# Kernel optimization log

Measured on AMD Instinct MI355X. Metric: run time of the kernel, lower is better.

The kernel has to match this reference:

```python
import jax, jax.numpy as jnp
import numpy as np

N_NODES = 100000
EMB_DIM = 128
HIDDEN = 128
N_EDGES = 1600000
N_LABEL = 200000


def _xavier(key, shape):
    fan_in, fan_out = shape[1], shape[0]
    lim = float(np.sqrt(6.0 / (fan_in + fan_out)))
    return jax.random.uniform(key, shape, jnp.float32, -lim, lim)


def setup_inputs() -> dict:
    key = jax.random.key(0)
    ks = jax.random.split(key, 8)
    n_id = jnp.arange(N_NODES, dtype=jnp.int64) if jax.config.jax_enable_x64 else jnp.arange(N_NODES, dtype=jnp.int32)
    edge_index = jax.random.randint(ks[0], (2, N_EDGES), 0, N_NODES)
    edge_label_index = jax.random.randint(ks[1], (2, N_LABEL), 0, N_NODES)
    emb_weight = _xavier(ks[2], (N_NODES, EMB_DIM))
    # layer 0: in=EMB_DIM -> HIDDEN ; layer 1: HIDDEN -> HIDDEN
    Wl0 = _xavier(ks[3], (HIDDEN, EMB_DIM))
    bl0 = jnp.zeros((HIDDEN,), jnp.float32)
    Wr0 = _xavier(ks[4], (HIDDEN, EMB_DIM))
    Wl1 = _xavier(ks[5], (HIDDEN, HIDDEN))
    bl1 = jnp.zeros((HIDDEN,), jnp.float32)
    Wr1 = _xavier(ks[6], (HIDDEN, HIDDEN))
    return {
        "n_id": n_id,
        "edge_index": edge_index,
        "edge_label_index": edge_label_index,
        "emb_weight": emb_weight,
        "Wl0": Wl0, "bl0": bl0, "Wr0": Wr0,
        "Wl1": Wl1, "bl1": bl1, "Wr1": Wr1,
    }


def _sage_conv(x, src, dst, Wl, bl, Wr, num_nodes):
    # PyG SAGEConv (aggr='mean'): out = lin_l(mean_{j in N(i)} x_j) + lin_r(x_i)
    agg = jax.ops.segment_sum(x[src], dst, num_segments=num_nodes)  # [N, D]
    deg = jax.ops.segment_sum(jnp.ones((src.shape[0],), x.dtype), dst, num_segments=num_nodes)
    mean = agg / jnp.maximum(deg, 1.0)[:, None]
    return mean @ Wl.T + bl + x @ Wr.T


def reference(n_id, edge_index, edge_label_index, emb_weight, Wl0, bl0, Wr0, Wl1, bl1, Wr1):
    src, dst = edge_index[0], edge_index[1]
    num_nodes = n_id.shape[0]
    x = emb_weight[n_id]                                  # [N, EMB_DIM]
    x = _sage_conv(x, src, dst, Wl0, bl0, Wr0, num_nodes)  # layer 0
    x = jax.nn.relu(x)                                     # relu between layers (dropout p=0, eval)
    z = _sage_conv(x, src, dst, Wl1, bl1, Wr1, num_nodes)  # layer 1 (no relu after last)
    s, d = edge_label_index[0], edge_label_index[1]
    return jnp.sum(z[s] * z[d], axis=-1)                   # [N_LABEL]
```

## Files before the change

### kernel.cpp

```cpp
#include <hip/hip_runtime.h>
#include <hip/hip_bf16.h>

typedef short bf16x8 __attribute__((ext_vector_type(8)));
typedef float f32x4 __attribute__((ext_vector_type(4)));
typedef float f32x2 __attribute__((ext_vector_type(2)));

#define BKT_SHIFT 9
#define BKT_RANGE 512
#define MAXBKT 256

__device__ __forceinline__ float bf2f(unsigned short u){
  union { unsigned int i; float f; } v; v.i = ((unsigned int)u)<<16; return v.f;
}
__device__ __forceinline__ unsigned short f2bf(float f){
  union { float f; unsigned int i; } v; v.f = f;
  unsigned int i = v.i;
  return (unsigned short)((i + 0x7fffu + ((i>>16)&1u)) >> 16);
}
__device__ __forceinline__ f32x2 up2(unsigned int v){
  union { unsigned int i; float f; } lo, hi;
  lo.i = v << 16; hi.i = v & 0xffff0000u;
  return (f32x2){lo.f, hi.f};
}

__global__ void k_zero(int* p, int n){
  int i = blockIdx.x*256 + threadIdx.x;
  if(i<n) p[i] = 0;
}

__global__ void k_bcount(const int* dst, int* gcount, int ne, int nbk){
  __shared__ int cnt[MAXBKT];
  int tid = threadIdx.x;
  if(tid < nbk) cnt[tid] = 0;
  __syncthreads();
  int base = blockIdx.x * 4096;
#pragma unroll
  for(int i=0;i<16;++i){
    int e = base + i*256 + tid;
    if(e < ne) atomicAdd(&cnt[dst[e] >> BKT_SHIFT], 1);
  }
  __syncthreads();
  if(tid < nbk && cnt[tid] > 0) atomicAdd(&gcount[tid], cnt[tid]);
}

__global__ void k_bscan(const int* gcount, int* gbase, int* gcursor, int nbk){
  __shared__ int sm[256];
  int t = threadIdx.x;
  int v = (t<nbk) ? gcount[t] : 0;
  sm[t] = v;
  __syncthreads();
  for(int off=1; off<256; off<<=1){
    int a = (t>=off) ? sm[t-off] : 0;
    __syncthreads();
    sm[t] += a;
    __syncthreads();
  }
  if(t<nbk){
    int excl = sm[t] - v;
    gbase[t] = excl;
    gcursor[t] = excl;
  }
}

__global__ void k_bscatter(const int* src, const int* dst, int* gcursor,
                           int2* ebuf, int ne, int nbk){
  __shared__ int cnt[MAXBKT];
  __shared__ int runbase[MAXBKT];
  int tid = threadIdx.x;
  if(tid < nbk) cnt[tid] = 0;
  __syncthreads();
  int base = blockIdx.x * 4096;
  int se[16], de[16], re[16];
#pragma unroll
  for(int i=0;i<16;++i){
    int e = base + i*256 + tid;
    if(e < ne){
      de[i] = dst[e];
      se[i] = src[e];
      re[i] = atomicAdd(&cnt[de[i] >> BKT_SHIFT], 1);
    } else de[i] = -1;
  }
  __syncthreads();
  if(tid < nbk) runbase[tid] = cnt[tid] ? atomicAdd(&gcursor[tid], cnt[tid]) : 0;
  __syncthreads();
#pragma unroll
  for(int i=0;i<16;++i){
    if(de[i] >= 0){
      int pos = runbase[de[i] >> BKT_SHIFT] + re[i];
      ebuf[pos] = make_int2(se[i], de[i]);
    }
  }
}

__global__ void k_bsort(const int2* ebuf, const int* gbase, const int* gcursor,
                        int* csr, int* row_off, int n, int ne, int nbk){
  __shared__ int h[BKT_RANGE];
  __shared__ int cur[BKT_RANGE];
  int t = threadIdx.x;
  int k = blockIdx.x;
  int lo = k << BKT_SHIFT;
  int beg = gbase[k], end = gcursor[k];
  h[t] = 0;
  __syncthreads();
  for(int e = beg + t; e < end; e += 512)
    atomicAdd(&h[ebuf[e].y - lo], 1);
  __syncthreads();
  int v = h[t];
  __shared__ int sm[512];
  sm[t] = v;
  __syncthreads();
  for(int off=1; off<512; off<<=1){
    int a = (t>=off) ? sm[t-off] : 0;
    __syncthreads();
    sm[t] += a;
    __syncthreads();
  }
  int excl = beg + sm[t] - v;
  cur[t] = excl;
  if(lo + t < n) row_off[lo + t] = excl;
  if(k == nbk-1 && t == 0) row_off[n] = ne;
  __syncthreads();
  for(int e = beg + t; e < end; e += 512){
    int2 sd = ebuf[e];
    int pos = atomicAdd(&cur[sd.y - lo], 1);
    csr[pos] = sd.x;
  }
}

__global__ void k_prep(const float* emb, const int* n_id, unsigned short* A0,
                       const float* Wl0, const float* Wr0, unsigned short* wc0,
                       const float* Wl1, const float* Wr1, unsigned short* wc1,
                       int n){
  int b = blockIdx.x;
  if(b < 256){
    const float* Wl = (b < 128) ? Wl0 : Wl1;
    const float* Wr = (b < 128) ? Wr0 : Wr1;
    unsigned short* wc = (b < 128) ? wc0 : wc1;
    int i = (b & 127)*256 + threadIdx.x;
    int nn = i >> 8, k = i & 255;
    float v = (k<128) ? Wl[nn*128 + k] : Wr[nn*128 + k - 128];
    wc[i] = f2bf(v);
  } else {
    int gid = (b-256)*256 + threadIdx.x;
    int row = gid >> 5, c4 = (gid & 31) * 4;
    if(row >= n) return;
    float4 v = *(const float4*)&emb[(long)n_id[row]*128 + c4];
    ushort4 o;
    o.x = f2bf(v.x); o.y = f2bf(v.y); o.z = f2bf(v.z); o.w = f2bf(v.w);
    *(ushort4*)&A0[(long)row*256 + 128 + c4] = o;
  }
}

__global__ void k_agg(const unsigned short* X, unsigned short* Mout,
                      const int* row_off, const int* csr, int n){
  int w = __builtin_amdgcn_readfirstlane((int)((blockIdx.x*blockDim.x + threadIdx.x) >> 6));
  int lane = threadIdx.x & 63;
  if(w >= n) return;
  int beg = row_off[w], end = row_off[w+1];
  int deg = end - beg;
  f32x2 acc = {0.f, 0.f};
  const char* Xb = (const char*)X + 256;
  int e = beg;
  for(; e + 8 <= end; e += 8){
    unsigned int v0 = ((const unsigned int*)(Xb + (long)csr[e  ]*512))[lane];
    unsigned int v1 = ((const unsigned int*)(Xb + (long)csr[e+1]*512))[lane];
    unsigned int v2 = ((const unsigned int*)(Xb + (long)csr[e+2]*512))[lane];
    unsigned int v3 = ((const unsigned int*)(Xb + (long)csr[e+3]*512))[lane];
    unsigned int v4 = ((const unsigned int*)(Xb + (long)csr[e+4]*512))[lane];
    unsigned int v5 = ((const unsigned int*)(Xb + (long)csr[e+5]*512))[lane];
    unsigned int v6 = ((const unsigned int*)(Xb + (long)csr[e+6]*512))[lane];
    unsigned int v7 = ((const unsigned int*)(Xb + (long)csr[e+7]*512))[lane];
    acc += up2(v0); acc += up2(v1); acc += up2(v2); acc += up2(v3);
    acc += up2(v4); acc += up2(v5); acc += up2(v6); acc += up2(v7);
  }
  for(; e + 4 <= end; e += 4){
    unsigned int v0 = ((const unsigned int*)(Xb + (long)csr[e  ]*512))[lane];
    unsigned int v1 = ((const unsigned int*)(Xb + (long)csr[e+1]*512))[lane];
    unsigned int v2 = ((const unsigned int*)(Xb + (long)csr[e+2]*512))[lane];
    unsigned int v3 = ((const unsigned int*)(Xb + (long)csr[e+3]*512))[lane];
    acc += up2(v0); acc += up2(v1); acc += up2(v2); acc += up2(v3);
  }
  for(; e < end; ++e){
    unsigned int v = ((const unsigned int*)(Xb + (long)csr[e]*512))[lane];
    acc += up2(v);
  }
  float inv = (deg>0) ? 1.0f/(float)deg : 0.f;
  float a0 = acc[0]*inv, a1 = acc[1]*inv;
  unsigned int o = ((unsigned int)f2bf(a1) << 16) | (unsigned int)f2bf(a0);
  *(unsigned int*)((char*)Mout + (long)w*512 + lane*4) = o;
}

template<int RELU, int OUTSTRIDE, int OUTOFF>
__global__ __launch_bounds__(256,2) void k_gemm(const unsigned short* A,
                                                const unsigned short* wc,
                                                const float* bias,
                                                unsigned short* out, int nrows){
  __shared__ unsigned short Wl[32768];
  int tid = threadIdx.x;
  for(int it=0; it<16; ++it){
    int idx  = it*256 + tid;
    int byte = idx*16;
    int row  = byte >> 9;
    int swz  = byte ^ ((row & 7) << 4);
    *(uint4*)((char*)Wl + swz) = *(const uint4*)((const char*)wc + byte);
  }
  __syncthreads();

  int lane = tid & 63, wv = tid >> 6;
  float bs[8];
#pragma unroll
  for(int nf=0; nf<8; ++nf) bs[nf] = bias[nf*16 + (lane & 15)];

  for(int t=0; t<4; ++t){
    int rowA = blockIdx.x*256 + t*64 + wv*16 + (lane & 15);
    int rcl  = rowA < nrows ? rowA : nrows-1;
    const char* Ab = (const char*)(A + (long)rcl*256) + ((lane>>4)*16);
    bf16x8 a[8];
#pragma unroll
    for(int k=0;k<8;++k) a[k] = *(const bf16x8*)(Ab + k*64);

    f32x4 acc[8];
#pragma unroll
    for(int i=0;i<8;++i) acc[i] = (f32x4){0.f,0.f,0.f,0.f};

#pragma unroll
    for(int nf=0; nf<8; ++nf){
      int rw = nf*16 + (lane & 15);
#pragma unroll
      for(int k=0;k<8;++k){
        int byte = (rw*512 + k*64 + (lane>>4)*16) ^ ((rw & 7) << 4);
        bf16x8 b = *(const bf16x8*)((const char*)Wl + byte);
        acc[nf] = __builtin_amdgcn_mfma_f32_16x16x32_bf16(a[k], b, acc[nf], 0, 0, 0);
      }
    }

    int rbase = blockIdx.x*256 + t*64 + wv*16 + (lane>>4)*4;
#pragma unroll
    for(int nf=0; nf<8; ++nf){
      int col = nf*16 + (lane & 15);
#pragma unroll
      for(int r=0;r<4;++r){
        int row = rbase + r;
        if(row < nrows){
          float v = acc[nf][r] + bs[nf];
          if(RELU) v = v > 0.f ? v : 0.f;
          out[(long)row*OUTSTRIDE + OUTOFF + col] = f2bf(v);
        }
      }
    }
  }
}

__global__ void k_dot(const unsigned short* z, const int* s, const int* d,
                      float* out, int nl){
  int wv = (blockIdx.x*256 + threadIdx.x) >> 6;
  int lane = threadIdx.x & 63;
  int g = lane >> 4;
  int gl = lane & 15;
  int pi = wv*4 + g;
  float acc = 0.f;
  if(pi < nl){
    int si = s[pi], di = d[pi];
    bf16x8 va = *(const bf16x8*)&z[(long)si*128 + gl*8];
    bf16x8 vb = *(const bf16x8*)&z[(long)di*128 + gl*8];
#pragma unroll
    for(int i=0;i<8;++i)
      acc += bf2f((unsigned short)va[i]) * bf2f((unsigned short)vb[i]);
#pragma unroll
    for(int off=1; off<16; off<<=1)
      acc += __shfl_xor(acc, off, 16);
    if(gl==0) out[pi] = acc;
  }
}

extern "C" void kernel_launch(void* const* d_in, const int* in_sizes, int n_in,
                              void* d_out, int out_size, void* d_ws, size_t ws_size,
                              hipStream_t stream){
  const int N  = in_sizes[0];
  const int NE = in_sizes[1] / 2;
  const int NL = in_sizes[2] / 2;
  const int*   n_id = (const int*)d_in[0];
  const int*   src  = (const int*)d_in[1];
  const int*   dst  = src + NE;
  const int*   ls   = (const int*)d_in[2];
  const int*   ld   = ls + NL;
  const float* emb  = (const float*)d_in[3];
  const float* Wl0  = (const float*)d_in[4];
  const float* bl0  = (const float*)d_in[5];
  const float* Wr0  = (const float*)d_in[6];
  const float* Wl1  = (const float*)d_in[7];
  const float* bl1  = (const float*)d_in[8];
  const float* Wr1  = (const float*)d_in[9];
  float* out = (float*)d_out;

  char* ws = (char*)d_ws;
  size_t off = 0;
  auto alloc = [&](size_t bytes)->char*{
    char* p = ws + off;
    off = (off + bytes + 255) & ~(size_t)255;
    return p;
  };
  unsigned short* A0   = (unsigned short*)alloc((size_t)N*256*2);
  unsigned short* A1   = (unsigned short*)alloc((size_t)N*256*2);
  int* row_off         = (int*)alloc((size_t)(N+1)*4);
  int* csr             = (int*)alloc((size_t)NE*4);
  int* gcount          = (int*)alloc(MAXBKT*4);
  int* gbase           = (int*)alloc(MAXBKT*4);
  int* gcursor         = (int*)alloc(MAXBKT*4);
  unsigned short* wc0  = (unsigned short*)alloc(128*256*2);
  unsigned short* wc1  = (unsigned short*)alloc(128*256*2);
  int2* ebuf           = (int2*)A1;
  unsigned short* Z    = A0;

  const int NBK = (N + BKT_RANGE - 1) >> BKT_SHIFT;
  const int NCH = (NE + 4095) / 4096;

  hipLaunchKernelGGL(k_zero,     dim3(1),            dim3(256), 0, stream, gcount, NBK);
  hipLaunchKernelGGL(k_bcount,   dim3(NCH),          dim3(256), 0, stream, dst, gcount, NE, NBK);
  hipLaunchKernelGGL(k_bscan,    dim3(1),            dim3(256), 0, stream, gcount, gbase, gcursor, NBK);
  hipLaunchKernelGGL(k_bscatter, dim3(NCH),          dim3(256), 0, stream, src, dst, gcursor, ebuf, NE, NBK);
  hipLaunchKernelGGL(k_bsort,    dim3(NBK),          dim3(512), 0, stream, ebuf, gbase, gcursor, csr, row_off, N, NE, NBK);
  hipLaunchKernelGGL(k_prep,     dim3(256 + (N*32+255)/256), dim3(256), 0, stream,
                     emb, n_id, A0, Wl0, Wr0, wc0, Wl1, Wr1, wc1, N);
  hipLaunchKernelGGL(k_agg,      dim3((N*64+255)/256),dim3(256), 0, stream, A0, A0, row_off, csr, N);
  hipLaunchKernelGGL((k_gemm<1,256,128>), dim3((N+255)/256), dim3(256), 0, stream, A0, wc0, bl0, A1, N);
  hipLaunchKernelGGL(k_agg,      dim3((N*64+255)/256),dim3(256), 0, stream, A1, A1, row_off, csr, N);
  hipLaunchKernelGGL((k_gemm<0,128,0>),   dim3((N+255)/256), dim3(256), 0, stream, A1, wc1, bl1, Z, N);
  hipLaunchKernelGGL(k_dot,      dim3((NL+15)/16),   dim3(256), 0, stream, Z, ls, ld, out, NL);
}
```

Measured before the change: 269.9 us.

## Pack sort edges into 32 bits and gather four neighbours per wave in aggregation

The bucket sort now stores each edge as a single 32-bit word, holding the source in the low 17 bits and the in-bucket destination offset above them, which halves the scratch traffic between scatter and sort. The aggregation kernel splits each wave into four 16-lane groups. Each group loads a whole 256-byte row with 16-byte vector loads, and the partial sums are then combined with cross-lane shuffles, aiming for more memory parallelism per neighbour. Zero-degree rows exit early, the tail is handled with clamped indices and zero weights, and the zeroing kernel is replaced by hipMemsetAsync. The packing assumes node ids fit in 17 bits, and the masked tail adds redundant loads.

```diff
diff --git a/kernel.cpp b/kernel.cpp
--- a/kernel.cpp
+++ b/kernel.cpp
@@ -17,15 +17,11 @@
   unsigned int i = v.i;
   return (unsigned short)((i + 0x7fffu + ((i>>16)&1u)) >> 16);
 }
-__device__ __forceinline__ f32x2 up2(unsigned int v){
+__device__ __forceinline__ void accfma(f32x2& a, unsigned int v, float m){
   union { unsigned int i; float f; } lo, hi;
   lo.i = v << 16; hi.i = v & 0xffff0000u;
-  return (f32x2){lo.f, hi.f};
-}
-
-__global__ void k_zero(int* p, int n){
-  int i = blockIdx.x*256 + threadIdx.x;
-  if(i<n) p[i] = 0;
+  a[0] = fmaf(lo.f, m, a[0]);
+  a[1] = fmaf(hi.f, m, a[1]);
 }
 
 __global__ void k_bcount(const int* dst, int* gcount, int ne, int nbk){
@@ -63,36 +59,34 @@
 }
 
 __global__ void k_bscatter(const int* src, const int* dst, int* gcursor,
-                           int2* ebuf, int ne, int nbk){
+                           unsigned int* ebuf, int ne, int nbk){
   __shared__ int cnt[MAXBKT];
   __shared__ int runbase[MAXBKT];
   int tid = threadIdx.x;
   if(tid < nbk) cnt[tid] = 0;
   __syncthreads();
   int base = blockIdx.x * 4096;
-  int se[16], de[16], re[16];
+  int pk[16], bk[16], re[16];
 #pragma unroll
   for(int i=0;i<16;++i){
     int e = base + i*256 + tid;
     if(e < ne){
-      de[i] = dst[e];
-      se[i] = src[e];
-      re[i] = atomicAdd(&cnt[de[i] >> BKT_SHIFT], 1);
-    } else de[i] = -1;
+      int d = dst[e];
+      bk[i] = d >> BKT_SHIFT;
+      pk[i] = (unsigned)src[e] | ((unsigned)(d & (BKT_RANGE-1)) << 17);
+      re[i] = atomicAdd(&cnt[bk[i]], 1);
+    } else bk[i] = -1;
   }
   __syncthreads();
   if(tid < nbk) runbase[tid] = cnt[tid] ? atomicAdd(&gcursor[tid], cnt[tid]) : 0;
   __syncthreads();
 #pragma unroll
   for(int i=0;i<16;++i){
-    if(de[i] >= 0){
-      int pos = runbase[de[i] >> BKT_SHIFT] + re[i];
-      ebuf[pos] = make_int2(se[i], de[i]);
-    }
-  }
-}
-
-__global__ void k_bsort(const int2* ebuf, const int* gbase, const int* gcursor,
+    if(bk[i] >= 0) ebuf[runbase[bk[i]] + re[i]] = pk[i];
+  }
+}
+
+__global__ void k_bsort(const unsigned int* ebuf, const int* gbase, const int* gcursor,
                         int* csr, int* row_off, int n, int ne, int nbk){
   __shared__ int h[BKT_RANGE];
   __shared__ int cur[BKT_RANGE];
@@ -103,7 +97,7 @@
   h[t] = 0;
   __syncthreads();
   for(int e = beg + t; e < end; e += 512)
-    atomicAdd(&h[ebuf[e].y - lo], 1);
+    atomicAdd(&h[ebuf[e] >> 17], 1);
   __syncthreads();
   int v = h[t];
   __shared__ int sm[512];
@@ -121,9 +115,9 @@
   if(k == nbk-1 && t == 0) row_off[n] = ne;
   __syncthreads();
   for(int e = beg + t; e < end; e += 512){
-    int2 sd = ebuf[e];
-    int pos = atomicAdd(&cur[sd.y - lo], 1);
-    csr[pos] = sd.x;
+    unsigned int p = ebuf[e];
+    int pos = atomicAdd(&cur[p >> 17], 1);
+    csr[pos] = (int)(p & 0x1FFFFu);
   }
 }
 
@@ -151,43 +145,54 @@
   }
 }
 
+__device__ __forceinline__ void do_quad(const char* Xb, const int* csr,
+                                        int ebase, int last, int g, int gl,
+                                        f32x2& a0, f32x2& a1, f32x2& a2, f32x2& a3){
+  int i0 = ebase   > last ? last : ebase;
+  int i1 = ebase+1 > last ? last : ebase+1;
+  int i2 = ebase+2 > last ? last : ebase+2;
+  int i3 = ebase+3 > last ? last : ebase+3;
+  int c0 = csr[i0], c1 = csr[i1], c2 = csr[i2], c3 = csr[i3];
+  int cg = g==0 ? c0 : g==1 ? c1 : g==2 ? c2 : c3;
+  float m = (ebase + g <= last) ? 1.f : 0.f;
+  const uint4 v = *(const uint4*)(Xb + (long)cg*512 + gl*16);
+  accfma(a0, v.x, m); accfma(a1, v.y, m); accfma(a2, v.z, m); accfma(a3, v.w, m);
+}
+
 __global__ void k_agg(const unsigned short* X, unsigned short* Mout,
                       const int* row_off, const int* csr, int n){
   int w = __builtin_amdgcn_readfirstlane((int)((blockIdx.x*blockDim.x + threadIdx.x) >> 6));
   int lane = threadIdx.x & 63;
+  int g = lane >> 4, gl = lane & 15;
   if(w >= n) return;
   int beg = row_off[w], end = row_off[w+1];
   int deg = end - beg;
-  f32x2 acc = {0.f, 0.f};
+  if(deg == 0){
+    if(g == 0) *(uint4*)((char*)Mout + (long)w*512 + gl*16) = (uint4){0,0,0,0};
+    return;
+  }
   const char* Xb = (const char*)X + 256;
-  int e = beg;
-  for(; e + 8 <= end; e += 8){
-    unsigned int v0 = ((const unsigned int*)(Xb + (long)csr[e  ]*512))[lane];
-    unsigned int v1 = ((const unsigned int*)(Xb + (long)csr[e+1]*512))[lane];
-    unsigned int v2 = ((const unsigned int*)(Xb + (long)csr[e+2]*512))[lane];
-    unsigned int v3 = ((const unsigned int*)(Xb + (long)csr[e+3]*512))[lane];
-    unsigned int v4 = ((const unsigned int*)(Xb + (long)csr[e+4]*512))[lane];
-    unsigned int v5 = ((const unsigned int*)(Xb + (long)csr[e+5]*512))[lane];
-    unsigned int v6 = ((const unsigned int*)(Xb + (long)csr[e+6]*512))[lane];
-    unsigned int v7 = ((const unsigned int*)(Xb + (long)csr[e+7]*512))[lane];
-    acc += up2(v0); acc += up2(v1); acc += up2(v2); acc += up2(v3);
-    acc += up2(v4); acc += up2(v5); acc += up2(v6); acc += up2(v7);
-  }
-  for(; e + 4 <= end; e += 4){
-    unsigned int v0 = ((const unsigned int*)(Xb + (long)csr[e  ]*512))[lane];
-    unsigned int v1 = ((const unsigned int*)(Xb + (long)csr[e+1]*512))[lane];
-    unsigned int v2 = ((const unsigned int*)(Xb + (long)csr[e+2]*512))[lane];
-    unsigned int v3 = ((const unsigned int*)(Xb + (long)csr[e+3]*512))[lane];
-    acc += up2(v0); acc += up2(v1); acc += up2(v2); acc += up2(v3);
-  }
-  for(; e < end; ++e){
-    unsigned int v = ((const unsigned int*)(Xb + (long)csr[e]*512))[lane];
-    acc += up2(v);
-  }
-  float inv = (deg>0) ? 1.0f/(float)deg : 0.f;
-  float a0 = acc[0]*inv, a1 = acc[1]*inv;
-  unsigned int o = ((unsigned int)f2bf(a1) << 16) | (unsigned int)f2bf(a0);
-  *(unsigned int*)((char*)Mout + (long)w*512 + lane*4) = o;
+  f32x2 a0={0.f,0.f}, a1={0.f,0.f}, a2={0.f,0.f}, a3={0.f,0.f};
+  int last = end - 1;
+  for(int e = beg; e < end; e += 16){
+    do_quad(Xb, csr, e,    last, g, gl, a0, a1, a2, a3);
+    do_quad(Xb, csr, e+4,  last, g, gl, a0, a1, a2, a3);
+    do_quad(Xb, csr, e+8,  last, g, gl, a0, a1, a2, a3);
+    do_quad(Xb, csr, e+12, last, g, gl, a0, a1, a2, a3);
+  }
+#pragma unroll
+  for(int off=16; off<=32; off<<=1){
+    a0[0] += __shfl_xor(a0[0], off); a0[1] += __shfl_xor(a0[1], off);
+    a1[0] += __shfl_xor(a1[0], off); a1[1] += __shfl_xor(a1[1], off);
+    a2[0] += __shfl_xor(a2[0], off); a2[1] += __shfl_xor(a2[1], off);
+    a3[0] += __shfl_xor(a3[0], off); a3[1] += __shfl_xor(a3[1], off);
+  }
+  float inv = 1.0f/(float)deg;
+  unsigned int o0 = ((unsigned)f2bf(a0[1]*inv) << 16) | f2bf(a0[0]*inv);
+  unsigned int o1 = ((unsigned)f2bf(a1[1]*inv) << 16) | f2bf(a1[0]*inv);
+  unsigned int o2 = ((unsigned)f2bf(a2[1]*inv) << 16) | f2bf(a2[0]*inv);
+  unsigned int o3 = ((unsigned)f2bf(a3[1]*inv) << 16) | f2bf(a3[0]*inv);
+  if(g == 0) *(uint4*)((char*)Mout + (long)w*512 + gl*16) = (uint4){o0,o1,o2,o3};
 }
 
 template<int RELU, int OUTSTRIDE, int OUTOFF>
@@ -309,13 +314,13 @@
   int* gcursor         = (int*)alloc(MAXBKT*4);
   unsigned short* wc0  = (unsigned short*)alloc(128*256*2);
   unsigned short* wc1  = (unsigned short*)alloc(128*256*2);
-  int2* ebuf           = (int2*)A1;
+  unsigned int* ebuf   = (unsigned int*)A1;
   unsigned short* Z    = A0;
 
   const int NBK = (N + BKT_RANGE - 1) >> BKT_SHIFT;
   const int NCH = (NE + 4095) / 4096;
 
-  hipLaunchKernelGGL(k_zero,     dim3(1),            dim3(256), 0, stream, gcount, NBK);
+  hipMemsetAsync(gcount, 0, NBK*4, stream);
   hipLaunchKernelGGL(k_bcount,   dim3(NCH),          dim3(256), 0, stream, dst, gcount, NE, NBK);
   hipLaunchKernelGGL(k_bscan,    dim3(1),            dim3(256), 0, stream, gcount, gbase, gcursor, NBK);
   hipLaunchKernelGGL(k_bscatter, dim3(NCH),          dim3(256), 0, stream, src, dst, gcursor, ebuf, NE, NBK);
```

Result: no change. 273.0 us (+1.2%).

## Fuse bucket scan into scatter/sort, pack edges to 32-bit, merge prep kernel

Applied to the files above, without the earlier changes.

Removes the zero and scan kernels by using a memset and recomputing the bucket prefix sum redundantly inside the scatter and sort kernels. The scatter kernel also absorbs the embedding/weight prep work as extra blocks, and edge records are packed into one 32-bit word (src in 17 bits, local dst offset in the upper bits) instead of int2. This cuts launch count and halves the intermediate edge buffer traffic. The cost is redundant per-block scans, and the packing assumes node ids fit in 17 bits.

```diff
diff --git a/kernel.cpp b/kernel.cpp
--- a/kernel.cpp
+++ b/kernel.cpp
@@ -23,11 +23,6 @@
   return (f32x2){lo.f, hi.f};
 }
 
-__global__ void k_zero(int* p, int n){
-  int i = blockIdx.x*256 + threadIdx.x;
-  if(i<n) p[i] = 0;
-}
-
 __global__ void k_bcount(const int* dst, int* gcount, int ne, int nbk){
   __shared__ int cnt[MAXBKT];
   int tid = threadIdx.x;
@@ -43,70 +38,95 @@
   if(tid < nbk && cnt[tid] > 0) atomicAdd(&gcount[tid], cnt[tid]);
 }
 
-__global__ void k_bscan(const int* gcount, int* gbase, int* gcursor, int nbk){
-  __shared__ int sm[256];
-  int t = threadIdx.x;
-  int v = (t<nbk) ? gcount[t] : 0;
-  sm[t] = v;
-  __syncthreads();
-  for(int off=1; off<256; off<<=1){
-    int a = (t>=off) ? sm[t-off] : 0;
-    __syncthreads();
-    sm[t] += a;
-    __syncthreads();
-  }
-  if(t<nbk){
-    int excl = sm[t] - v;
-    gbase[t] = excl;
-    gcursor[t] = excl;
-  }
-}
-
-__global__ void k_bscatter(const int* src, const int* dst, int* gcursor,
-                           int2* ebuf, int ne, int nbk){
+__global__ void k_bscatter_prep(const int* src, const int* dst, const int* gcount,
+                                int* gcur0, unsigned int* ebuf, int ne, int nbk, int nch,
+                                const float* emb, const int* n_id, unsigned short* A0,
+                                const float* Wl0, const float* Wr0, unsigned short* wc0,
+                                const float* Wl1, const float* Wr1, unsigned short* wc1,
+                                int n){
+  int b = blockIdx.x;
+  int tid = threadIdx.x;
+  if(b >= nch){
+    int pb = b - nch;
+    if(pb < 256){
+      const float* Wl = (pb < 128) ? Wl0 : Wl1;
+      const float* Wr = (pb < 128) ? Wr0 : Wr1;
+      unsigned short* wc = (pb < 128) ? wc0 : wc1;
+      int i = (pb & 127)*256 + tid;
+      int nn = i >> 8, k = i & 255;
+      float v = (k<128) ? Wl[nn*128 + k] : Wr[nn*128 + k - 128];
+      wc[i] = f2bf(v);
+    } else {
+      int gid = (pb-256)*256 + tid;
+      int row = gid >> 5, c4 = (gid & 31) * 4;
+      if(row >= n) return;
+      float4 v = *(const float4*)&emb[(long)n_id[row]*128 + c4];
+      ushort4 o;
+      o.x = f2bf(v.x); o.y = f2bf(v.y); o.z = f2bf(v.z); o.w = f2bf(v.w);
+      *(ushort4*)&A0[(long)row*256 + 128 + c4] = o;
+    }
+    return;
+  }
   __shared__ int cnt[MAXBKT];
   __shared__ int runbase[MAXBKT];
-  int tid = threadIdx.x;
-  if(tid < nbk) cnt[tid] = 0;
-  __syncthreads();
-  int base = blockIdx.x * 4096;
-  int se[16], de[16], re[16];
+  __shared__ int sg[MAXBKT];
+  cnt[tid] = 0;
+  sg[tid] = (tid < nbk) ? gcount[tid] : 0;
+  __syncthreads();
+  int base = b * 4096;
+  int pk[16], bk[16], re[16];
 #pragma unroll
   for(int i=0;i<16;++i){
     int e = base + i*256 + tid;
     if(e < ne){
-      de[i] = dst[e];
-      se[i] = src[e];
-      re[i] = atomicAdd(&cnt[de[i] >> BKT_SHIFT], 1);
-    } else de[i] = -1;
-  }
-  __syncthreads();
-  if(tid < nbk) runbase[tid] = cnt[tid] ? atomicAdd(&gcursor[tid], cnt[tid]) : 0;
+      int d = dst[e];
+      bk[i] = d >> BKT_SHIFT;
+      pk[i] = (unsigned)src[e] | ((unsigned)(d & (BKT_RANGE-1)) << 17);
+      re[i] = atomicAdd(&cnt[bk[i]], 1);
+    } else bk[i] = -1;
+  }
+  int myv = sg[tid];
+  __syncthreads();
+  for(int off=1; off<256; off<<=1){
+    int a = (tid>=off) ? sg[tid-off] : 0;
+    __syncthreads();
+    sg[tid] += a;
+    __syncthreads();
+  }
+  if(tid < nbk)
+    runbase[tid] = (sg[tid] - myv) + (cnt[tid] ? atomicAdd(&gcur0[tid], cnt[tid]) : 0);
   __syncthreads();
 #pragma unroll
   for(int i=0;i<16;++i){
-    if(de[i] >= 0){
-      int pos = runbase[de[i] >> BKT_SHIFT] + re[i];
-      ebuf[pos] = make_int2(se[i], de[i]);
-    }
-  }
-}
-
-__global__ void k_bsort(const int2* ebuf, const int* gbase, const int* gcursor,
+    if(bk[i] >= 0) ebuf[runbase[bk[i]] + re[i]] = pk[i];
+  }
+}
+
+__global__ void k_bsort(const unsigned int* ebuf, const int* gcount,
                         int* csr, int* row_off, int n, int ne, int nbk){
+  __shared__ int sg[MAXBKT];
   __shared__ int h[BKT_RANGE];
   __shared__ int cur[BKT_RANGE];
+  __shared__ int sm[512];
   int t = threadIdx.x;
   int k = blockIdx.x;
+  if(t < MAXBKT) sg[t] = (t < nbk) ? gcount[t] : 0;
+  __syncthreads();
+  for(int off=1; off<256; off<<=1){
+    int a = (t>=off && t<256) ? sg[t-off] : 0;
+    __syncthreads();
+    if(t<256) sg[t] += a;
+    __syncthreads();
+  }
+  int beg = sg[k] - gcount[k];
+  int end = sg[k];
   int lo = k << BKT_SHIFT;
-  int beg = gbase[k], end = gcursor[k];
   h[t] = 0;
   __syncthreads();
   for(int e = beg + t; e < end; e += 512)
-    atomicAdd(&h[ebuf[e].y - lo], 1);
+    atomicAdd(&h[ebuf[e] >> 17], 1);
   __syncthreads();
   int v = h[t];
-  __shared__ int sm[512];
   sm[t] = v;
   __syncthreads();
   for(int off=1; off<512; off<<=1){
@@ -121,33 +141,9 @@
   if(k == nbk-1 && t == 0) row_off[n] = ne;
   __syncthreads();
   for(int e = beg + t; e < end; e += 512){
-    int2 sd = ebuf[e];
-    int pos = atomicAdd(&cur[sd.y - lo], 1);
-    csr[pos] = sd.x;
-  }
-}
-
-__global__ void k_prep(const float* emb, const int* n_id, unsigned short* A0,
-                       const float* Wl0, const float* Wr0, unsigned short* wc0,
-                       const float* Wl1, const float* Wr1, unsigned short* wc1,
-                       int n){
-  int b = blockIdx.x;
-  if(b < 256){
-    const float* Wl = (b < 128) ? Wl0 : Wl1;
-    const float* Wr = (b < 128) ? Wr0 : Wr1;
-    unsigned short* wc = (b < 128) ? wc0 : wc1;
-    int i = (b & 127)*256 + threadIdx.x;
-    int nn = i >> 8, k = i & 255;
-    float v = (k<128) ? Wl[nn*128 + k] : Wr[nn*128 + k - 128];
-    wc[i] = f2bf(v);
-  } else {
-    int gid = (b-256)*256 + threadIdx.x;
-    int row = gid >> 5, c4 = (gid & 31) * 4;
-    if(row >= n) return;
-    float4 v = *(const float4*)&emb[(long)n_id[row]*128 + c4];
-    ushort4 o;
-    o.x = f2bf(v.x); o.y = f2bf(v.y); o.z = f2bf(v.z); o.w = f2bf(v.w);
-    *(ushort4*)&A0[(long)row*256 + 128 + c4] = o;
+    unsigned int p = ebuf[e];
+    int pos = atomicAdd(&cur[p >> 17], 1);
+    csr[pos] = (int)(p & 0x1FFFFu);
   }
 }
 
@@ -304,27 +300,26 @@
   unsigned short* A1   = (unsigned short*)alloc((size_t)N*256*2);
   int* row_off         = (int*)alloc((size_t)(N+1)*4);
   int* csr             = (int*)alloc((size_t)NE*4);
-  int* gcount          = (int*)alloc(MAXBKT*4);
-  int* gbase           = (int*)alloc(MAXBKT*4);
-  int* gcursor         = (int*)alloc(MAXBKT*4);
+  int* gcount          = (int*)alloc(MAXBKT*4*2);
+  int* gcur0           = gcount + MAXBKT;
   unsigned short* wc0  = (unsigned short*)alloc(128*256*2);
   unsigned short* wc1  = (unsigned short*)alloc(128*256*2);
-  int2* ebuf           = (int2*)A1;
+  unsigned int* ebuf   = (unsigned int*)A1;
   unsigned short* Z    = A0;
 
   const int NBK = (N + BKT_RANGE - 1) >> BKT_SHIFT;
   const int NCH = (NE + 4095) / 4096;
 
-  hipLaunchKernelGGL(k_zero,     dim3(1),            dim3(256), 0, stream, gcount, NBK);
-  hipLaunchKernelGGL(k_bcount,   dim3(NCH),          dim3(256), 0, stream, dst, gcount, NE, NBK);
-  hipLaunchKernelGGL(k_bscan,    dim3(1),            dim3(256), 0, stream, gcount, gbase, gcursor, NBK);
-  hipLaunchKernelGGL(k_bscatter, dim3(NCH),          dim3(256), 0, stream, src, dst, gcursor, ebuf, NE, NBK);
-  hipLaunchKernelGGL(k_bsort,    dim3(NBK),          dim3(512), 0, stream, ebuf, gbase, gcursor, csr, row_off, N, NE, NBK);
-  hipLaunchKernelGGL(k_prep,     dim3(256 + (N*32+255)/256), dim3(256), 0, stream,
+  hipMemsetAsync(gcount, 0, MAXBKT*4*2, stream);
+  hipLaunchKernelGGL(k_bcount, dim3(NCH), dim3(256), 0, stream, dst, gcount, NE, NBK);
+  hipLaunchKernelGGL(k_bscatter_prep, dim3(NCH + 256 + (N*32+255)/256), dim3(256), 0, stream,
+                     src, dst, gcount, gcur0, ebuf, NE, NBK, NCH,
                      emb, n_id, A0, Wl0, Wr0, wc0, Wl1, Wr1, wc1, N);
-  hipLaunchKernelGGL(k_agg,      dim3((N*64+255)/256),dim3(256), 0, stream, A0, A0, row_off, csr, N);
+  hipLaunchKernelGGL(k_bsort, dim3(NBK), dim3(512), 0, stream,
+                     ebuf, gcount, csr, row_off, N, NE, NBK);
+  hipLaunchKernelGGL(k_agg, dim3((N*64+255)/256), dim3(256), 0, stream, A0, A0, row_off, csr, N);
   hipLaunchKernelGGL((k_gemm<1,256,128>), dim3((N+255)/256), dim3(256), 0, stream, A0, wc0, bl0, A1, N);
-  hipLaunchKernelGGL(k_agg,      dim3((N*64+255)/256),dim3(256), 0, stream, A1, A1, row_off, csr, N);
-  hipLaunchKernelGGL((k_gemm<0,128,0>),   dim3((N+255)/256), dim3(256), 0, stream, A1, wc1, bl1, Z, N);
-  hipLaunchKernelGGL(k_dot,      dim3((NL+15)/16),   dim3(256), 0, stream, Z, ls, ld, out, NL);
-}
+  hipLaunchKernelGGL(k_agg, dim3((N*64+255)/256), dim3(256), 0, stream, A1, A1, row_off, csr, N);
+  hipLaunchKernelGGL((k_gemm<0,128,0>), dim3((N+255)/256), dim3(256), 0, stream, A1, wc1, bl1, Z, N);
+  hipLaunchKernelGGL(k_dot, dim3((NL+15)/16), dim3(256), 0, stream, Z, ls, ld, out, NL);
+}
```

Measured after the change: 260.2 us (median of 2 runs). -3.6%, faster.
